# Optimization experiments

Measured on AMD Instinct MI355X. Metric: run time of the kernel, lower is better.

The kernel has to match this reference:

```python
import jax, jax.numpy as jnp
import numpy as np

N_NODES = 100000


def _gcn_conv(x, edge_index, W, b):
    """PyG GCNConv: add self-loops, symmetric deg^-1/2 normalization, scatter-add."""
    N = x.shape[0]
    h = x @ W  # [N, out]
    src = edge_index[0]
    dst = edge_index[1]
    loop = jnp.arange(N, dtype=src.dtype)
    src = jnp.concatenate([src, loop])
    dst = jnp.concatenate([dst, loop])
    deg = jax.ops.segment_sum(jnp.ones(src.shape[0], dtype=h.dtype), dst, num_segments=N)
    dinv = jnp.where(deg > 0, jax.lax.rsqrt(deg), 0.0)
    norm = dinv[src] * dinv[dst]  # [E+N]
    msgs = h[src] * norm[:, None]  # gather + scale
    out = jax.ops.segment_sum(msgs, dst, num_segments=N)  # scatter-add
    return out + b


def setup_inputs() -> dict:
    key = jax.random.key(0)
    k1, k2, k3, k4 = jax.random.split(key, 4)
    F_IN, H = 512, 16
    x = jax.random.normal(k1, (N_NODES, F_IN), dtype=jnp.float32)
    edge_index = jax.random.randint(k2, (2, 3200000), 0, N_NODES, dtype=jnp.int64)
    # Glorot init like PyG GCNConv
    lim = np.sqrt(6.0 / (F_IN + H)).astype(np.float32)
    W1 = jax.random.uniform(k3, (F_IN, H), dtype=jnp.float32, minval=-lim, maxval=lim)
    b1 = jnp.zeros((H,), dtype=jnp.float32)
    return {"x": x, "edge_index": edge_index, "W1": W1, "b1": b1}


def reference(x, edge_index, W1, b1):
    # forward: relu(GCNConv(x)); dropout is identity in eval; log_softmax over features
    h = jax.nn.relu(_gcn_conv(x, edge_index, W1, b1))
    return jax.nn.log_softmax(h, axis=1)
```

## Files before the change

kernel.cpp:

```cpp
#include <hip/hip_runtime.h>
#include <hip/hip_bf16.h>
#include <stdint.h>

#define N_NODES 100000
#define F_IN    512
#define HOUT    16

#define BSH   8
#define NBUK  391
#define CAP   9216
#define CHUNK 8192

typedef __attribute__((ext_vector_type(8))) short bf16x8;
typedef __attribute__((ext_vector_type(4))) float f32x4;

__device__ __forceinline__ short f2bf(float f) {
    union { float f; uint32_t u; } v; v.f = f;
    uint32_t r = (v.u + 0x7FFFu + ((v.u >> 16) & 1u)) >> 16;
    return (short)r;
}
__device__ __forceinline__ float bf2f(uint32_t bits16) {
    union { uint32_t u; float f; } v; v.u = bits16 << 16;
    return v.f;
}

__global__ void k_detect(const uint32_t* __restrict__ e_u32, uint32_t* __restrict__ flag) {
    if (blockIdx.x == 0 && threadIdx.x == 0) {
        uint32_t o = 0;
        #pragma unroll
        for (int i = 1; i < 32; i += 2) o |= e_u32[i];
        flag[0] = (o == 0u) ? 1u : 0u;
    }
}

__device__ __forceinline__ int edge_at(const void* ei, int64_t idx, uint32_t is64) {
    if (is64) return (int)((const long long*)ei)[idx];
    return ((const int*)ei)[idx];
}

__global__ __launch_bounds__(512) void k_binA(const void* __restrict__ ei, int E,
                                              const uint32_t* __restrict__ flag,
                                              uint32_t* __restrict__ bucket_woff,
                                              uint32_t* __restrict__ gpairs) {
    const uint32_t is64 = flag[0];
    const int t = threadIdx.x;
    const int base = blockIdx.x * CHUNK;
    const int chunk_n = min(CHUNK, E - base);

    __shared__ uint32_t h[512];
    __shared__ uint32_t ex[512];
    __shared__ uint32_t pcnt[512];
    __shared__ uint32_t gbase[512];
    __shared__ uint32_t sorted[CHUNK];
    __shared__ uint16_t sbuck[CHUNK];

    h[t] = 0;
    __syncthreads();

    uint32_t pr[16];
    uint16_t bk[16];
    #pragma unroll
    for (int k = 0; k < 16; ++k) {
        int e = base + k * 512 + t;
        bk[k] = 0xFFFFu;
        if (e < E) {
            uint32_t s = (uint32_t)edge_at(ei, e, is64);
            uint32_t d = (uint32_t)edge_at(ei, (int64_t)E + e, is64);
            uint32_t b = d >> BSH;
            pr[k] = (s << BSH) | (d & ((1u << BSH) - 1u));
            bk[k] = (uint16_t)b;
            atomicAdd(&h[b], 1u);
        }
    }
    __syncthreads();

    const uint32_t hv = h[t];
    for (int off = 1; off < 512; off <<= 1) {
        uint32_t v = (t >= off) ? h[t - off] : 0u;
        __syncthreads();
        h[t] += v;
        __syncthreads();
    }
    ex[t] = h[t] - hv;
    pcnt[t] = ex[t];
    if (t < NBUK) gbase[t] = atomicAdd(&bucket_woff[t], hv);
    __syncthreads();

    #pragma unroll
    for (int k = 0; k < 16; ++k) {
        if (bk[k] != 0xFFFFu) {
            uint32_t slot = atomicAdd(&pcnt[bk[k]], 1u);
            sorted[slot] = pr[k];
            sbuck[slot] = bk[k];
        }
    }
    __syncthreads();

    #pragma unroll
    for (int k = 0; k < 16; ++k) {
        int i = k * 512 + t;
        if (i < chunk_n) {
            uint32_t b = sbuck[i];
            uint32_t pos = gbase[b] + ((uint32_t)i - ex[b]);
            gpairs[(size_t)b * CAP + pos] = sorted[i];
        }
    }
}

__global__ __launch_bounds__(256) void k_hist(const uint32_t* __restrict__ bucket_woff,
                                              const uint32_t* __restrict__ gpairs,
                                              uint32_t* __restrict__ cnt) {
    const int b = blockIdx.x;
    const int t = threadIdx.x;
    const uint32_t count = bucket_woff[b];
    const uint32_t* gp = gpairs + (size_t)b * CAP;

    __shared__ uint32_t lc[256];
    lc[t] = 0;
    __syncthreads();
    for (uint32_t i = t; i < count; i += 256)
        atomicAdd(&lc[gp[i] & 255u], 1u);
    __syncthreads();
    int gn = (b << BSH) + t;
    if (gn < N_NODES) cnt[gn] = lc[t];
}

__global__ __launch_bounds__(256) void k_gemm(const float* __restrict__ x,
                                              const float* __restrict__ W,
                                              const uint32_t* __restrict__ cnt,
                                              ushort* __restrict__ hsb) {
    const int lane = threadIdx.x & 63;
    const int wid  = threadIdx.x >> 6;
    const int tile = blockIdx.x * 4 + wid;
    if (tile * 16 >= N_NODES) return;
    const int c    = lane & 15;
    const int half = lane >> 4;

    bf16x8 bfrag[16];
    #pragma unroll
    for (int s = 0; s < 16; ++s) {
        #pragma unroll
        for (int e = 0; e < 8; ++e) {
            int k = 32 * s + 8 * half + e;
            bfrag[s][e] = f2bf(W[k * HOUT + c]);
        }
    }

    const int row = tile * 16 + c;
    const float* xr = x + (int64_t)row * F_IN;
    f32x4 acc = {0.f, 0.f, 0.f, 0.f};
    #pragma unroll
    for (int s = 0; s < 16; ++s) {
        const float4 a0 = *(const float4*)(xr + 32 * s + 8 * half);
        const float4 a1 = *(const float4*)(xr + 32 * s + 8 * half + 4);
        bf16x8 af;
        af[0] = f2bf(a0.x); af[1] = f2bf(a0.y); af[2] = f2bf(a0.z); af[3] = f2bf(a0.w);
        af[4] = f2bf(a1.x); af[5] = f2bf(a1.y); af[6] = f2bf(a1.z); af[7] = f2bf(a1.w);
        acc = __builtin_amdgcn_mfma_f32_16x16x32_bf16(af, bfrag[s], acc, 0, 0, 0);
    }

    #pragma unroll
    for (int r = 0; r < 4; ++r) {
        int orow = tile * 16 + 4 * half + r;
        float dinv = rsqrtf((float)(cnt[orow] + 1u));
        hsb[(int64_t)orow * HOUT + c] = (ushort)f2bf(acc[r] * dinv);
    }
}

__global__ __launch_bounds__(512) void k_sortagg(const uint32_t* __restrict__ bucket_woff,
                                                 const uint32_t* __restrict__ gpairs,
                                                 const uint32_t* __restrict__ cnt,
                                                 const ushort* __restrict__ hsb,
                                                 const float* __restrict__ bias,
                                                 float* __restrict__ out) {
    const int bk = blockIdx.x;
    const int t = threadIdx.x;
    const uint32_t count = bucket_woff[bk];
    const uint32_t* gp = gpairs + (size_t)bk * CAP;

    __shared__ uint32_t lc[256];
    __shared__ uint32_t st[256];
    __shared__ uint32_t cur[256];
    __shared__ uint32_t sc[256];
    __shared__ uint32_t lsrc[CAP];

    if (t < 256) {
        int gn = (bk << BSH) + t;
        lc[t] = (gn < N_NODES) ? cnt[gn] : 0u;
        sc[t] = lc[t];
    }
    __syncthreads();
    for (int off = 1; off < 256; off <<= 1) {
        uint32_t v = 0;
        if (t < 256 && t >= off) v = sc[t - off];
        __syncthreads();
        if (t < 256) sc[t] += v;
        __syncthreads();
    }
    if (t < 256) {
        st[t] = sc[t] - lc[t];
        cur[t] = st[t];
    }
    __syncthreads();

    for (uint32_t i = t; i < count; i += 512) {
        uint32_t p = gp[i];
        uint32_t pos = atomicAdd(&cur[p & 255u], 1u);
        lsrc[pos] = p >> BSH;
    }
    __syncthreads();

    const int f = t & 15;
    const int g = t >> 4;
    const float bf = bias[f];

    #pragma unroll
    for (int i = 0; i < 8; ++i) {
        int dl = g + 32 * i;
        int gn = (bk << BSH) + dl;
        if (gn >= N_NODES) break;
        const uint32_t s0 = st[dl];
        const uint32_t n  = lc[dl];

        float acc = 0.f;
        uint32_t j = 0;
        for (; j + 4 <= n; j += 4) {
            uint32_t a = lsrc[s0 + j], b2 = lsrc[s0 + j + 1];
            uint32_t c2 = lsrc[s0 + j + 2], d2 = lsrc[s0 + j + 3];
            float v0 = bf2f(hsb[(size_t)a  * HOUT + f]);
            float v1 = bf2f(hsb[(size_t)b2 * HOUT + f]);
            float v2 = bf2f(hsb[(size_t)c2 * HOUT + f]);
            float v3 = bf2f(hsb[(size_t)d2 * HOUT + f]);
            acc += (v0 + v1) + (v2 + v3);
        }
        for (; j < n; ++j)
            acc += bf2f(hsb[(size_t)lsrc[s0 + j] * HOUT + f]);

        const float dinv = rsqrtf((float)(n + 1u));
        const float self = bf2f(hsb[(size_t)gn * HOUT + f]);
        float v = fmaxf(fmaf(dinv, acc + self, bf), 0.f);

        float m = v;
        #pragma unroll
        for (int d = 1; d < 16; d <<= 1) m = fmaxf(m, __shfl_xor(m, d));
        float ex = __expf(v - m);
        float sum = ex;
        #pragma unroll
        for (int d = 1; d < 16; d <<= 1) sum += __shfl_xor(sum, d);
        out[(size_t)gn * HOUT + f] = v - (m + __logf(sum));
    }
}

extern "C" void kernel_launch(void* const* d_in, const int* in_sizes, int n_in,
                              void* d_out, int out_size, void* d_ws, size_t ws_size,
                              hipStream_t stream) {
    const float* x  = (const float*)d_in[0];
    const void*  ei = d_in[1];
    const float* W  = (const float*)d_in[2];
    const float* b  = (const float*)d_in[3];
    float* out = (float*)d_out;
    const int E = in_sizes[1] / 2;

    char* ws = (char*)d_ws;
    uint32_t* flag        = (uint32_t*)ws;
    uint32_t* bucket_woff = (uint32_t*)(ws + 1024);
    uint32_t* gpairs      = (uint32_t*)(ws + (1 << 20));
    ushort*   hsb         = (ushort*)(ws + (16 << 20));
    uint32_t* cnt         = (uint32_t*)(ws + (20 << 20));

    hipMemsetAsync(bucket_woff, 0, NBUK * sizeof(uint32_t), stream);

    k_detect<<<1, 64, 0, stream>>>((const uint32_t*)ei, flag);
    k_binA<<<(E + CHUNK - 1) / CHUNK, 512, 0, stream>>>(ei, E, flag, bucket_woff, gpairs);
    k_hist<<<NBUK, 256, 0, stream>>>(bucket_woff, gpairs, cnt);
    k_gemm<<<(6250 + 3) / 4, 256, 0, stream>>>(x, W, cnt, hsb);
    k_sortagg<<<NBUK, 512, 0, stream>>>(bucket_woff, gpairs, cnt, hsb, b, out);
}
```

Measured before the change: 120.1 us.

## Co-schedule edge binning and GEMM in one launch, apply degree scaling afterward

Merges the edge-binning kernel and the x@W MFMA GEMM into a single launch that uses block-index ranges to pick the role, so the memory-bound GEMM can overlap with binning instead of waiting on degree counts. The GEMM now writes unscaled fp32 rows to a new scratch buffer. A combined histogram-and-scale kernel then applies deg^-1/2 and converts to bf16. The memset and detect kernel are folded into one init kernel. This costs an extra fp32 round trip of h (about 6.4 MB written and read) and gives the fused kernel heavier shared-memory use for the GEMM blocks, which may limit occupancy.

Result: faster. 112.2 us (-6.6%).

```diff
diff --git a/kernel.cpp b/kernel.cpp
--- a/kernel.cpp
+++ b/kernel.cpp
@@ -10,6 +10,7 @@
 #define NBUK  391
 #define CAP   9216
 #define CHUNK 8192
+#define GEMM_BLOCKS 782
 
 typedef __attribute__((ext_vector_type(8))) short bf16x8;
 typedef __attribute__((ext_vector_type(4))) float f32x4;
@@ -24,29 +25,30 @@
     return v.f;
 }
 
-__global__ void k_detect(const uint32_t* __restrict__ e_u32, uint32_t* __restrict__ flag) {
-    if (blockIdx.x == 0 && threadIdx.x == 0) {
-        uint32_t o = 0;
-        #pragma unroll
-        for (int i = 1; i < 32; i += 2) o |= e_u32[i];
-        flag[0] = (o == 0u) ? 1u : 0u;
-    }
-}
-
 __device__ __forceinline__ int edge_at(const void* ei, int64_t idx, uint32_t is64) {
     if (is64) return (int)((const long long*)ei)[idx];
     return ((const int*)ei)[idx];
 }
 
-__global__ __launch_bounds__(512) void k_binA(const void* __restrict__ ei, int E,
-                                              const uint32_t* __restrict__ flag,
-                                              uint32_t* __restrict__ bucket_woff,
-                                              uint32_t* __restrict__ gpairs) {
-    const uint32_t is64 = flag[0];
+__global__ void k_init(const uint32_t* __restrict__ e_u32, uint32_t* __restrict__ flag,
+                       uint32_t* __restrict__ bucket_woff) {
     const int t = threadIdx.x;
-    const int base = blockIdx.x * CHUNK;
-    const int chunk_n = min(CHUNK, E - base);
-
+    if (t < NBUK) bucket_woff[t] = 0u;
+    if (t == 0) {
+        uint32_t o = 0;
+        #pragma unroll
+        for (int i = 1; i < 32; i += 2) o |= e_u32[i];
+        flag[0] = (o == 0u) ? 1u : 0u;
+    }
+}
+
+__global__ __launch_bounds__(512) void k_fused(const void* __restrict__ ei, int E, int nchunks,
+                                               const uint32_t* __restrict__ flag,
+                                               uint32_t* __restrict__ bucket_woff,
+                                               uint32_t* __restrict__ gpairs,
+                                               const float* __restrict__ x,
+                                               const float* __restrict__ W,
+                                               float* __restrict__ hs) {
     __shared__ uint32_t h[512];
     __shared__ uint32_t ex[512];
     __shared__ uint32_t pcnt[512];
@@ -54,62 +56,108 @@
     __shared__ uint32_t sorted[CHUNK];
     __shared__ uint16_t sbuck[CHUNK];
 
-    h[t] = 0;
-    __syncthreads();
-
-    uint32_t pr[16];
-    uint16_t bk[16];
-    #pragma unroll
-    for (int k = 0; k < 16; ++k) {
-        int e = base + k * 512 + t;
-        bk[k] = 0xFFFFu;
-        if (e < E) {
-            uint32_t s = (uint32_t)edge_at(ei, e, is64);
-            uint32_t d = (uint32_t)edge_at(ei, (int64_t)E + e, is64);
-            uint32_t b = d >> BSH;
-            pr[k] = (s << BSH) | (d & ((1u << BSH) - 1u));
-            bk[k] = (uint16_t)b;
-            atomicAdd(&h[b], 1u);
-        }
-    }
-    __syncthreads();
-
-    const uint32_t hv = h[t];
-    for (int off = 1; off < 512; off <<= 1) {
-        uint32_t v = (t >= off) ? h[t - off] : 0u;
-        __syncthreads();
-        h[t] += v;
-        __syncthreads();
-    }
-    ex[t] = h[t] - hv;
-    pcnt[t] = ex[t];
-    if (t < NBUK) gbase[t] = atomicAdd(&bucket_woff[t], hv);
-    __syncthreads();
-
-    #pragma unroll
-    for (int k = 0; k < 16; ++k) {
-        if (bk[k] != 0xFFFFu) {
-            uint32_t slot = atomicAdd(&pcnt[bk[k]], 1u);
-            sorted[slot] = pr[k];
-            sbuck[slot] = bk[k];
-        }
-    }
-    __syncthreads();
-
-    #pragma unroll
-    for (int k = 0; k < 16; ++k) {
-        int i = k * 512 + t;
-        if (i < chunk_n) {
-            uint32_t b = sbuck[i];
-            uint32_t pos = gbase[b] + ((uint32_t)i - ex[b]);
-            gpairs[(size_t)b * CAP + pos] = sorted[i];
-        }
-    }
-}
-
-__global__ __launch_bounds__(256) void k_hist(const uint32_t* __restrict__ bucket_woff,
-                                              const uint32_t* __restrict__ gpairs,
-                                              uint32_t* __restrict__ cnt) {
+    const int t = threadIdx.x;
+
+    if ((int)blockIdx.x < nchunks) {
+        const uint32_t is64 = flag[0];
+        const int base = blockIdx.x * CHUNK;
+        const int chunk_n = min(CHUNK, E - base);
+
+        h[t] = 0;
+        __syncthreads();
+
+        uint32_t pr[16];
+        uint16_t bk[16];
+        #pragma unroll
+        for (int k = 0; k < 16; ++k) {
+            int e = base + k * 512 + t;
+            bk[k] = 0xFFFFu;
+            if (e < E) {
+                uint32_t s = (uint32_t)edge_at(ei, e, is64);
+                uint32_t d = (uint32_t)edge_at(ei, (int64_t)E + e, is64);
+                uint32_t b = d >> BSH;
+                pr[k] = (s << BSH) | (d & ((1u << BSH) - 1u));
+                bk[k] = (uint16_t)b;
+                atomicAdd(&h[b], 1u);
+            }
+        }
+        __syncthreads();
+
+        const uint32_t hv = h[t];
+        for (int off = 1; off < 512; off <<= 1) {
+            uint32_t v = (t >= off) ? h[t - off] : 0u;
+            __syncthreads();
+            h[t] += v;
+            __syncthreads();
+        }
+        ex[t] = h[t] - hv;
+        pcnt[t] = ex[t];
+        if (t < NBUK) gbase[t] = atomicAdd(&bucket_woff[t], hv);
+        __syncthreads();
+
+        #pragma unroll
+        for (int k = 0; k < 16; ++k) {
+            if (bk[k] != 0xFFFFu) {
+                uint32_t slot = atomicAdd(&pcnt[bk[k]], 1u);
+                sorted[slot] = pr[k];
+                sbuck[slot] = bk[k];
+            }
+        }
+        __syncthreads();
+
+        #pragma unroll
+        for (int k = 0; k < 16; ++k) {
+            int i = k * 512 + t;
+            if (i < chunk_n) {
+                uint32_t b = sbuck[i];
+                uint32_t pos = gbase[b] + ((uint32_t)i - ex[b]);
+                gpairs[(size_t)b * CAP + pos] = sorted[i];
+            }
+        }
+    } else {
+        const int lane = t & 63;
+        const int wid  = t >> 6;
+        const int tile = ((int)blockIdx.x - nchunks) * 8 + wid;
+        if (tile * 16 >= N_NODES) return;
+        const int c    = lane & 15;
+        const int half = lane >> 4;
+
+        bf16x8 bfrag[16];
+        #pragma unroll
+        for (int s = 0; s < 16; ++s) {
+            #pragma unroll
+            for (int e = 0; e < 8; ++e) {
+                int k = 32 * s + 8 * half + e;
+                bfrag[s][e] = f2bf(W[k * HOUT + c]);
+            }
+        }
+
+        const int row = tile * 16 + c;
+        const float* xr = x + (int64_t)row * F_IN;
+        f32x4 acc = {0.f, 0.f, 0.f, 0.f};
+        #pragma unroll
+        for (int s = 0; s < 16; ++s) {
+            const float4 a0 = *(const float4*)(xr + 32 * s + 8 * half);
+            const float4 a1 = *(const float4*)(xr + 32 * s + 8 * half + 4);
+            bf16x8 af;
+            af[0] = f2bf(a0.x); af[1] = f2bf(a0.y); af[2] = f2bf(a0.z); af[3] = f2bf(a0.w);
+            af[4] = f2bf(a1.x); af[5] = f2bf(a1.y); af[6] = f2bf(a1.z); af[7] = f2bf(a1.w);
+            acc = __builtin_amdgcn_mfma_f32_16x16x32_bf16(af, bfrag[s], acc, 0, 0, 0);
+        }
+
+        #pragma unroll
+        for (int r = 0; r < 4; ++r) {
+            int orow = tile * 16 + 4 * half + r;
+            hs[(int64_t)orow * HOUT + c] = acc[r];
+        }
+    }
+}
+
+__global__ __launch_bounds__(256) void k_histscale(const uint32_t* __restrict__ bucket_woff,
+                                                   const uint32_t* __restrict__ gpairs,
+                                                   const float* __restrict__ hs,
+                                                   uint32_t* __restrict__ cnt,
+                                                   ushort* __restrict__ hsb) {
     const int b = blockIdx.x;
     const int t = threadIdx.x;
     const uint32_t count = bucket_woff[b];
@@ -121,49 +169,24 @@
     for (uint32_t i = t; i < count; i += 256)
         atomicAdd(&lc[gp[i] & 255u], 1u);
     __syncthreads();
-    int gn = (b << BSH) + t;
-    if (gn < N_NODES) cnt[gn] = lc[t];
-}
-
-__global__ __launch_bounds__(256) void k_gemm(const float* __restrict__ x,
-                                              const float* __restrict__ W,
-                                              const uint32_t* __restrict__ cnt,
-                                              ushort* __restrict__ hsb) {
-    const int lane = threadIdx.x & 63;
-    const int wid  = threadIdx.x >> 6;
-    const int tile = blockIdx.x * 4 + wid;
-    if (tile * 16 >= N_NODES) return;
-    const int c    = lane & 15;
-    const int half = lane >> 4;
-
-    bf16x8 bfrag[16];
-    #pragma unroll
-    for (int s = 0; s < 16; ++s) {
-        #pragma unroll
-        for (int e = 0; e < 8; ++e) {
-            int k = 32 * s + 8 * half + e;
-            bfrag[s][e] = f2bf(W[k * HOUT + c]);
-        }
-    }
-
-    const int row = tile * 16 + c;
-    const float* xr = x + (int64_t)row * F_IN;
-    f32x4 acc = {0.f, 0.f, 0.f, 0.f};
-    #pragma unroll
-    for (int s = 0; s < 16; ++s) {
-        const float4 a0 = *(const float4*)(xr + 32 * s + 8 * half);
-        const float4 a1 = *(const float4*)(xr + 32 * s + 8 * half + 4);
-        bf16x8 af;
-        af[0] = f2bf(a0.x); af[1] = f2bf(a0.y); af[2] = f2bf(a0.z); af[3] = f2bf(a0.w);
-        af[4] = f2bf(a1.x); af[5] = f2bf(a1.y); af[6] = f2bf(a1.z); af[7] = f2bf(a1.w);
-        acc = __builtin_amdgcn_mfma_f32_16x16x32_bf16(af, bfrag[s], acc, 0, 0, 0);
-    }
-
-    #pragma unroll
-    for (int r = 0; r < 4; ++r) {
-        int orow = tile * 16 + 4 * half + r;
-        float dinv = rsqrtf((float)(cnt[orow] + 1u));
-        hsb[(int64_t)orow * HOUT + c] = (ushort)f2bf(acc[r] * dinv);
+
+    const int gn = (b << BSH) + t;
+    if (gn < N_NODES) {
+        const uint32_t deg = lc[t];
+        cnt[gn] = deg;
+        const float dinv = rsqrtf((float)(deg + 1u));
+        const float4* hr = (const float4*)(hs + (size_t)gn * HOUT);
+        ushort o[16];
+        #pragma unroll
+        for (int q = 0; q < 4; ++q) {
+            float4 v = hr[q];
+            o[4*q + 0] = (ushort)f2bf(v.x * dinv);
+            o[4*q + 1] = (ushort)f2bf(v.y * dinv);
+            o[4*q + 2] = (ushort)f2bf(v.z * dinv);
+            o[4*q + 3] = (ushort)f2bf(v.w * dinv);
+        }
+        ulonglong4* ow = (ulonglong4*)(hsb + (size_t)gn * HOUT);
+        *ow = *(const ulonglong4*)o;
     }
 }
 
@@ -260,6 +283,7 @@
     const float* b  = (const float*)d_in[3];
     float* out = (float*)d_out;
     const int E = in_sizes[1] / 2;
+    const int nchunks = (E + CHUNK - 1) / CHUNK;
 
     char* ws = (char*)d_ws;
     uint32_t* flag        = (uint32_t*)ws;
@@ -267,12 +291,11 @@
     uint32_t* gpairs      = (uint32_t*)(ws + (1 << 20));
     ushort*   hsb         = (ushort*)(ws + (16 << 20));
     uint32_t* cnt         = (uint32_t*)(ws + (20 << 20));
-
-    hipMemsetAsync(bucket_woff, 0, NBUK * sizeof(uint32_t), stream);
-
-    k_detect<<<1, 64, 0, stream>>>((const uint32_t*)ei, flag);
-    k_binA<<<(E + CHUNK - 1) / CHUNK, 512, 0, stream>>>(ei, E, flag, bucket_woff, gpairs);
-    k_hist<<<NBUK, 256, 0, stream>>>(bucket_woff, gpairs, cnt);
-    k_gemm<<<(6250 + 3) / 4, 256, 0, stream>>>(x, W, cnt, hsb);
+    float*    hs          = (float*)(ws + (21 << 20));
+
+    k_init<<<1, 512, 0, stream>>>((const uint32_t*)ei, flag, bucket_woff);
+    k_fused<<<nchunks + GEMM_BLOCKS, 512, 0, stream>>>(ei, E, nchunks, flag,
+                                                       bucket_woff, gpairs, x, W, hs);
+    k_histscale<<<NBUK, 256, 0, stream>>>(bucket_woff, gpairs, hs, cnt, hsb);
     k_sortagg<<<NBUK, 512, 0, stream>>>(bucket_woff, gpairs, cnt, hsb, b, out);
 }
```
